# Kernel optimization log

Measured on AMD Instinct MI355X. Metric: run time of the kernel, lower is better.

The kernel has to match this reference:

```python
import jax, jax.numpy as jnp
import numpy as np

N, E = 50000, 800000
IN_C, HID, HEADS, LAT = 128, 64, 2, 32
NEG_SLOPE = 0.2  # PyG GATConv default LeakyReLU slope


def gat_layer(x, src, dst, W, att_src, att_dst, bias, heads, out_ch, concat, n):
    # Linear projection, per-head: [n, heads, out_ch]
    h = (x @ W).reshape(n, heads, out_ch)
    a_src = jnp.einsum('nhc,hc->nh', h, att_src)  # [n, heads]
    a_dst = jnp.einsum('nhc,hc->nh', h, att_dst)
    # Per-edge attention logits (edge j->i uses src j, dst i)
    alpha = jax.nn.leaky_relu(a_src[src] + a_dst[dst], negative_slope=NEG_SLOPE)  # [e, heads]
    # Segment softmax over incoming edges of each destination node
    amax = jax.ops.segment_max(alpha, dst, num_segments=n)
    ealpha = jnp.exp(alpha - amax[dst])
    denom = jax.ops.segment_sum(ealpha, dst, num_segments=n)
    alpha = ealpha / (denom[dst] + 1e-16)
    # Weighted scatter-aggregate of source features
    msg = h[src] * alpha[:, :, None]  # [e, heads, out_ch]
    out = jax.ops.segment_sum(msg, dst, num_segments=n)  # [n, heads, out_ch]
    out = out.reshape(n, heads * out_ch) if concat else out.mean(axis=1)
    return out + bias


def setup_inputs() -> dict:
    key = jax.random.key(0)
    ks = jax.random.split(key, 16)
    x = jax.random.normal(ks[0], (N, IN_C), dtype=jnp.float32)
    edge_index = jax.random.randint(ks[1], (2, E), 0, N, dtype=jnp.int32).astype(jnp.int64)
    s = 0.1
    W1 = jax.random.normal(ks[2], (IN_C, HEADS * HID), dtype=jnp.float32) * s
    att_src1 = jax.random.normal(ks[3], (HEADS, HID), dtype=jnp.float32) * s
    att_dst1 = jax.random.normal(ks[4], (HEADS, HID), dtype=jnp.float32) * s
    b1 = jnp.zeros((HEADS * HID,), dtype=jnp.float32)
    Wmu = jax.random.normal(ks[5], (HEADS * HID, LAT), dtype=jnp.float32) * s
    att_src_mu = jax.random.normal(ks[6], (1, LAT), dtype=jnp.float32) * s
    att_dst_mu = jax.random.normal(ks[7], (1, LAT), dtype=jnp.float32) * s
    bmu = jnp.zeros((LAT,), dtype=jnp.float32)
    Wlv = jax.random.normal(ks[8], (HEADS * HID, LAT), dtype=jnp.float32) * s
    att_src_lv = jax.random.normal(ks[9], (1, LAT), dtype=jnp.float32) * s
    att_dst_lv = jax.random.normal(ks[10], (1, LAT), dtype=jnp.float32) * s
    blv = jnp.zeros((LAT,), dtype=jnp.float32)
    return {"x": x, "edge_index": edge_index, "W1": W1, "att_src1": att_src1,
            "att_dst1": att_dst1, "b1": b1, "Wmu": Wmu, "att_src_mu": att_src_mu,
            "att_dst_mu": att_dst_mu, "bmu": bmu, "Wlv": Wlv,
            "att_src_lv": att_src_lv, "att_dst_lv": att_dst_lv, "blv": blv}


def reference(x, edge_index, W1, att_src1, att_dst1, b1,
              Wmu, att_src_mu, att_dst_mu, bmu,
              Wlv, att_src_lv, att_dst_lv, blv):
    n = x.shape[0]
    # PyG GATConv adds self-loops by default
    loops = jnp.arange(n, dtype=edge_index.dtype)
    src = jnp.concatenate([edge_index[0], loops])
    dst = jnp.concatenate([edge_index[1], loops])
    h = gat_layer(x, src, dst, W1, att_src1, att_dst1, b1, HEADS, HID, True, n)
    h = jax.nn.elu(h)
    mu = gat_layer(h, src, dst, Wmu, att_src_mu, att_dst_mu, bmu, 1, LAT, False, n)
    logvar = gat_layer(h, src, dst, Wlv, att_src_lv, att_dst_lv, blv, 1, LAT, False, n)
    return (mu, logvar)
```

## Files before the change

### kernel.cpp

```cpp
#include <hip/hip_runtime.h>
#include <hip/hip_bf16.h>

#define N_NODES 50000
#define N_EDGES 800000
#define EP (N_EDGES + N_NODES)
#define IN_C 128
#define HID 64
#define HEADS 2
#define LAT 32
#define NEG_SLOPE 0.2f
#define MAXDEG 256
#define MAXDEG1 96
#define NBUCKET 391
#define BCAP 3072
#define CHUNK 2048
#define NSCAT ((EP + CHUNK - 1) / CHUNK)
#define NPROJ1 ((N_NODES + 31) / 32)

typedef __attribute__((ext_vector_type(8))) short bf16x8;
typedef __attribute__((ext_vector_type(4))) float f32x4;

__device__ __forceinline__ unsigned short f2bf(float f) {
  unsigned u = __float_as_uint(f);
  u += 0x7FFF + ((u >> 16) & 1);
  return (unsigned short)(u >> 16);
}
__device__ __forceinline__ float bf_lo(unsigned u) { return __uint_as_float(u << 16); }
__device__ __forceinline__ float bf_hi(unsigned u) { return __uint_as_float(u & 0xFFFF0000u); }

__device__ __forceinline__ bf16x8 pack_bf8(const float* __restrict__ p) {
  float4 a = *(const float4*)p;
  float4 b = *(const float4*)(p + 4);
  bf16x8 r;
  r[0] = (short)f2bf(a.x); r[1] = (short)f2bf(a.y);
  r[2] = (short)f2bf(a.z); r[3] = (short)f2bf(a.w);
  r[4] = (short)f2bf(b.x); r[5] = (short)f2bf(b.y);
  r[6] = (short)f2bf(b.z); r[7] = (short)f2bf(b.w);
  return r;
}

__global__ __launch_bounds__(256) void prep_kernel(
    const float* __restrict__ W1, const float* __restrict__ Wmu,
    const float* __restrict__ Wlv, int* __restrict__ cursor,
    unsigned short* __restrict__ Wb1g, unsigned short* __restrict__ Wb2g) {
  const int b = blockIdx.x, t = threadIdx.x;
  if (b == 0) {
    for (int i = t; i < NBUCKET; i += 256) cursor[i] = 0;
  } else if (b <= 64) {
    int i = (b - 1) * 256 + t;
    int k = i >> 7, n = i & 127;
    int kk = k >> 5, q = (k >> 3) & 3, j = k & 7;
    Wb1g[((((kk << 2) + q) << 7) + n) * 8 + j] = f2bf(W1[i]);
  } else {
    int i = (b - 65) * 256 + t;
    int k = i >> 6, n = i & 63;
    float v = (n < 32) ? Wmu[k * 32 + n] : Wlv[k * 32 + (n - 32)];
    int kk = k >> 5, q = (k >> 3) & 3, j = k & 7;
    Wb2g[((((kk << 2) + q) << 6) + n) * 8 + j] = f2bf(v);
  }
}

struct ScatSmem {
  int histL[512];
  int baseL[512];
  int gbaseL[512];
  int wsumS[4];
  int nvalS;
  unsigned staging[CHUNK];
  unsigned short bktidL[CHUNK];
};
struct Proj1Smem {
  float part[32][4];
  unsigned short xs[32][136];
};
union K1Smem { ScatSmem sc; Proj1Smem p1; };

__global__ __launch_bounds__(256) void k1_kernel(
    const int* __restrict__ ei, int* __restrict__ cursor,
    unsigned* __restrict__ csr,
    const float* __restrict__ x, const unsigned short* __restrict__ Wb1g,
    const float* __restrict__ att_src, const float* __restrict__ att_dst,
    unsigned short* __restrict__ h1b, float* __restrict__ a1) {
  __shared__ K1Smem sm;
  const int t = threadIdx.x, lane = t & 63, wid = t >> 6;

  if (blockIdx.x < NSCAT) {
    for (int i = t; i < 512; i += 256) sm.sc.histL[i] = 0;
    __syncthreads();
    int myb[CHUNK / 256];
    int myloc[CHUNK / 256];
    unsigned mypay[CHUNK / 256];
    #pragma unroll
    for (int i = 0; i < CHUNK / 256; ++i) {
      int e = blockIdx.x * CHUNK + i * 256 + t;
      if (e < EP) {
        int s, d;
        if (e < N_EDGES) { s = ei[e]; d = ei[N_EDGES + e]; }
        else { s = d = e - N_EDGES; }
        int b = d >> 7;
        myb[i] = b;
        mypay[i] = ((unsigned)(d & 127) << 17) | (unsigned)s;
        myloc[i] = atomicAdd(&sm.sc.histL[b], 1);
      } else myb[i] = -1;
    }
    __syncthreads();
    {
      int v0 = sm.sc.histL[2 * t], v1 = sm.sc.histL[2 * t + 1];
      int pair = v0 + v1, inc = pair;
      #pragma unroll
      for (int off = 1; off < 64; off <<= 1) {
        int nv = __shfl_up(inc, off);
        if (lane >= off) inc += nv;
      }
      if (lane == 63) sm.sc.wsumS[wid] = inc;
      __syncthreads();
      if (t == 0) {
        int run = 0;
        #pragma unroll
        for (int w = 0; w < 4; ++w) { int c = sm.sc.wsumS[w]; sm.sc.wsumS[w] = run; run += c; }
        sm.sc.nvalS = run;
      }
      __syncthreads();
      int excl = sm.sc.wsumS[wid] + inc - pair;
      sm.sc.baseL[2 * t] = excl;
      sm.sc.baseL[2 * t + 1] = excl + v0;
    }
    __syncthreads();
    #pragma unroll
    for (int i = 0; i < CHUNK / 256; ++i)
      if (myb[i] >= 0) {
        int p = sm.sc.baseL[myb[i]] + myloc[i];
        sm.sc.staging[p] = mypay[i];
        sm.sc.bktidL[p] = (unsigned short)myb[i];
      }
    for (int b = t; b < NBUCKET; b += 256) {
      int c = sm.sc.histL[b];
      sm.sc.gbaseL[b] = c ? atomicAdd(&cursor[b], c) : 0;
    }
    __syncthreads();
    const int nval = sm.sc.nvalS;
    for (int j = t; j < nval; j += 256) {
      int b = sm.sc.bktidL[j];
      int off = sm.sc.gbaseL[b] + (j - sm.sc.baseL[b]);
      if (off < BCAP) csr[b * BCAP + off] = sm.sc.staging[j];
    }
  } else {
    const int pb = blockIdx.x - NSCAT;
    const int row0 = pb * 32;
    if (t < 128) ((float*)sm.p1.part)[t] = 0.f;
    {
      int row = t >> 3;
      int col0 = (t & 7) * 16;
      int gr = row0 + row; if (gr >= N_NODES) gr = N_NODES - 1;
      const float* xp = x + (size_t)gr * 128 + col0;
      *(bf16x8*)&sm.p1.xs[row][col0]     = pack_bf8(xp);
      *(bf16x8*)&sm.p1.xs[row][col0 + 8] = pack_bf8(xp + 8);
    }
    __syncthreads();
    const int w = wid;
    const int m = lane & 15, quad = lane >> 4;
    const int n0 = w * 32;
    const int head = w >> 1;
    f32x4 acc[2][2] = {};
    #pragma unroll
    for (int kk = 0; kk < 4; ++kk) {
      bf16x8 afr[2], bfr[2];
      #pragma unroll
      for (int mt = 0; mt < 2; ++mt)
        afr[mt] = *(const bf16x8*)&sm.p1.xs[mt * 16 + m][kk * 32 + quad * 8];
      #pragma unroll
      for (int nt = 0; nt < 2; ++nt)
        bfr[nt] = *(const bf16x8*)&Wb1g[((((kk << 2) + quad) << 7) + n0 + nt * 16 + m) * 8];
      #pragma unroll
      for (int mt = 0; mt < 2; ++mt)
        #pragma unroll
        for (int nt = 0; nt < 2; ++nt)
          acc[mt][nt] = __builtin_amdgcn_mfma_f32_16x16x32_bf16(
              afr[mt], bfr[nt], acc[mt][nt], 0, 0, 0);
    }
    float asv[2], adv[2];
    #pragma unroll
    for (int nt = 0; nt < 2; ++nt) {
      int cc = ((n0 & 63) + nt * 16 + m);
      asv[nt] = att_src[head * HID + cc];
      adv[nt] = att_dst[head * HID + cc];
    }
    #pragma unroll
    for (int mt = 0; mt < 2; ++mt)
      #pragma unroll
      for (int r = 0; r < 4; ++r) {
        int row = row0 + mt * 16 + quad * 4 + r;
        if (row < N_NODES) {
          #pragma unroll
          for (int nt = 0; nt < 2; ++nt)
            h1b[(size_t)row * 128 + n0 + nt * 16 + m] = f2bf(acc[mt][nt][r]);
        }
        float s = acc[mt][0][r] * asv[0] + acc[mt][1][r] * asv[1];
        float d = acc[mt][0][r] * adv[0] + acc[mt][1][r] * adv[1];
        #pragma unroll
        for (int off = 8; off; off >>= 1) {
          s += __shfl_xor(s, off);
          d += __shfl_xor(d, off);
        }
        if (m == 0) {
          atomicAdd(&sm.p1.part[mt * 16 + quad * 4 + r][head], s);
          atomicAdd(&sm.p1.part[mt * 16 + quad * 4 + r][2 + head], d);
        }
      }
    __syncthreads();
    if (t < 32) {
      int row = row0 + t;
      if (row < N_NODES)
        *(float4*)&a1[(size_t)row * 4] = make_float4(
            sm.p1.part[t][0], sm.p1.part[t][1], sm.p1.part[t][2], sm.p1.part[t][3]);
    }
  }
}

__global__ __launch_bounds__(256) void bucket_fill_kernel(
    const int* __restrict__ cursor, unsigned* __restrict__ csr,
    int* __restrict__ counts, int* __restrict__ cend) {
  __shared__ unsigned eseg[BCAP];
  __shared__ int hist[128];
  __shared__ int basef[128];
  __shared__ int cur[128];
  const int b = blockIdx.x, t = threadIdx.x;
  const int segbase = b * BCAP;
  int cnt = cursor[b];
  if (cnt > BCAP) cnt = BCAP;
  if (t < 128) hist[t] = 0;
  __syncthreads();
  for (int j = t; j < cnt; j += 256) {
    unsigned u = csr[segbase + j];
    eseg[j] = u;
    atomicAdd(&hist[u >> 17], 1);
  }
  __syncthreads();
  if (t < 64) {
    int v0 = hist[2 * t], v1 = hist[2 * t + 1];
    int pair = v0 + v1, inc = pair;
    #pragma unroll
    for (int off = 1; off < 64; off <<= 1) {
      int nv = __shfl_up(inc, off);
      if (t >= off) inc += nv;
    }
    int excl = inc - pair;
    basef[2 * t] = excl;
    basef[2 * t + 1] = excl + v0;
  }
  __syncthreads();
  if (t < 128) {
    cur[t] = basef[t];
    int n = b * 128 + t;
    if (n < N_NODES) {
      counts[n] = hist[t];
      cend[n] = segbase + basef[t] + hist[t];
    }
  }
  __syncthreads();
  for (int j = t; j < cnt; j += 256) {
    unsigned u = eseg[j];
    int dl = u >> 17;
    int p = atomicAdd(&cur[dl], 1);
    csr[segbase + p] = u & 0x1FFFF;
  }
}

__global__ __launch_bounds__(256) void agg1_proj2_kernel(
    const int* __restrict__ counts, const int* __restrict__ cend,
    const unsigned* __restrict__ csr_src, const float4* __restrict__ a1,
    const unsigned* __restrict__ h1b2, const float* __restrict__ b,
    const unsigned short* __restrict__ Wb2g,
    const float* __restrict__ asmu, const float* __restrict__ admu,
    const float* __restrict__ aslv, const float* __restrict__ adlv,
    unsigned short* __restrict__ h2b, float* __restrict__ a2) {
  __shared__ __align__(16) float2 w_lds[16][MAXDEG1];
  __shared__ __align__(16) unsigned short s_lds[16][MAXDEG1];
  __shared__ __align__(16) unsigned short hrow[16][136];
  __shared__ __align__(16) float sm_a2[16][4];
  const int t = threadIdx.x, wid = t >> 6, lane = t & 63;
  if (t < 64) ((float*)sm_a2)[t] = 0.f;
  const int nbase = blockIdx.x * 16;

  int cnt_r[4];
  float p0r[4], p1r[4];
  #pragma unroll
  for (int nd = 0; nd < 4; ++nd) {
    const int slot = wid * 4 + nd;
    const int n = nbase + slot;
    const int end = cend[n];
    int cnt = counts[n]; if (cnt > MAXDEG1) cnt = MAXDEG1;
    const int beg = end - cnt;
    cnt_r[nd] = cnt;
    const float4 bv = a1[n];
    float p0 = 0.f, p1 = 0.f;
    for (int i = lane; i < cnt; i += 64) {
      int s = (int)csr_src[beg + i];
      float4 av = a1[s];
      float l0 = av.x + bv.z; l0 = l0 > 0.f ? l0 : NEG_SLOPE * l0;
      float l1 = av.y + bv.w; l1 = l1 > 0.f ? l1 : NEG_SLOPE * l1;
      float e0 = __expf(l0), e1 = __expf(l1);
      w_lds[slot][i] = make_float2(e0, e1);
      s_lds[slot][i] = (unsigned short)s;
      p0 += e0; p1 += e1;
    }
    #pragma unroll
    for (int off = 32; off; off >>= 1) {
      p0 += __shfl_xor(p0, off);
      p1 += __shfl_xor(p1, off);
    }
    p0r[nd] = p0; p1r[nd] = p1;
  }

  const int g = lane >> 4, lq = lane & 15, head = lq >> 3;
  #pragma unroll
  for (int nd = 0; nd < 4; ++nd) {
    const int slot = wid * 4 + nd;
    const int cnt = cnt_r[nd];
    float acc[8] = {0.f, 0.f, 0.f, 0.f, 0.f, 0.f, 0.f, 0.f};
    #pragma unroll 4
    for (int i = g; i < cnt; i += 4) {
      int s = (int)s_lds[slot][i];
      float w = ((const float*)&w_lds[slot][i])[head];
      uint4 u = *(const uint4*)(h1b2 + (size_t)s * 64 + lq * 4);
      acc[0] += bf_lo(u.x) * w; acc[1] += bf_hi(u.x) * w;
      acc[2] += bf_lo(u.y) * w; acc[3] += bf_hi(u.y) * w;
      acc[4] += bf_lo(u.z) * w; acc[5] += bf_hi(u.z) * w;
      acc[6] += bf_lo(u.w) * w; acc[7] += bf_hi(u.w) * w;
    }
    #pragma unroll
    for (int jj = 0; jj < 8; ++jj) {
      acc[jj] += __shfl_xor(acc[jj], 16);
      acc[jj] += __shfl_xor(acc[jj], 32);
    }
    if (g == 0) {
      float inv = 1.f / ((head ? p1r[nd] : p0r[nd]) + 1e-16f);
      bf16x8 o;
      #pragma unroll
      for (int jj = 0; jj < 8; ++jj) {
        float v = acc[jj] * inv + b[lq * 8 + jj];
        v = v > 0.f ? v : (__expf(v) - 1.f);
        o[jj] = (short)f2bf(v);
      }
      *(bf16x8*)&hrow[slot][lq * 8] = o;
    }
  }
  __syncthreads();

  const int m = lane & 15, quad = lane >> 4;
  const int c = wid * 16 + m;
  const int j = wid >> 1;
  f32x4 acc2 = {};
  #pragma unroll
  for (int kk = 0; kk < 4; ++kk) {
    bf16x8 af = *(const bf16x8*)&hrow[m][kk * 32 + quad * 8];
    bf16x8 bf = *(const bf16x8*)&Wb2g[((((kk << 2) + quad) << 6) + c) * 8];
    acc2 = __builtin_amdgcn_mfma_f32_16x16x32_bf16(af, bf, acc2, 0, 0, 0);
  }
  const float asv = (j ? aslv : asmu)[(wid & 1) * 16 + m];
  const float adv = (j ? adlv : admu)[(wid & 1) * 16 + m];
  #pragma unroll
  for (int r = 0; r < 4; ++r) {
    const int slot = quad * 4 + r;
    h2b[(size_t)(nbase + slot) * 64 + c] = f2bf(acc2[r]);
    float s = acc2[r] * asv, d = acc2[r] * adv;
    #pragma unroll
    for (int off = 8; off; off >>= 1) {
      s += __shfl_xor(s, off);
      d += __shfl_xor(d, off);
    }
    if (m == 0) {
      atomicAdd(&sm_a2[slot][j * 2 + 0], s);
      atomicAdd(&sm_a2[slot][j * 2 + 1], d);
    }
  }
  __syncthreads();
  if (t < 16)
    *(float4*)&a2[(size_t)(nbase + t) * 4] = make_float4(
        sm_a2[t][0], sm_a2[t][1], sm_a2[t][2], sm_a2[t][3]);
}

__global__ __launch_bounds__(256) void agg2_csr_kernel(
    const int* __restrict__ counts, const int* __restrict__ cend,
    const unsigned* __restrict__ csr_src, const float4* __restrict__ a2,
    const unsigned* __restrict__ h2b2,
    const float* __restrict__ bmu, const float* __restrict__ blv,
    float* __restrict__ out) {
  __shared__ float2 w_lds[4][MAXDEG];
  __shared__ int   s_lds[4][MAXDEG];
  const int t = threadIdx.x, wid = t >> 6, lane = t & 63;
  const int n = blockIdx.x * 4 + wid;
  const int end = cend[n];
  int cnt = counts[n];
  if (cnt > MAXDEG) cnt = MAXDEG;
  const int beg = end - cnt;
  const float4 bv = a2[n];
  float p0 = 0.f, p1 = 0.f;
  for (int i = lane; i < cnt; i += 64) {
    int s = (int)csr_src[beg + i];
    float4 av = a2[s];
    float l0 = av.x + bv.y; l0 = l0 > 0.f ? l0 : NEG_SLOPE * l0;
    float l1 = av.z + bv.w; l1 = l1 > 0.f ? l1 : NEG_SLOPE * l1;
    float e0 = expf(l0), e1 = expf(l1);
    w_lds[wid][i] = make_float2(e0, e1);
    s_lds[wid][i] = s;
    p0 += e0; p1 += e1;
  }
  #pragma unroll
  for (int off = 32; off; off >>= 1) {
    p0 += __shfl_xor(p0, off);
    p1 += __shfl_xor(p1, off);
  }
  __syncthreads();
  const int g = lane >> 3;
  const int lq = lane & 7;
  const int j = lq >> 2;
  float acc[8] = {0.f, 0.f, 0.f, 0.f, 0.f, 0.f, 0.f, 0.f};
  #pragma unroll 2
  for (int i = g; i < cnt; i += 8) {
    int s = s_lds[wid][i];
    float w = ((const float*)&w_lds[wid][i])[j];
    uint4 u = *(const uint4*)(h2b2 + (size_t)s * 32 + lq * 4);
    acc[0] += bf_lo(u.x) * w; acc[1] += bf_hi(u.x) * w;
    acc[2] += bf_lo(u.y) * w; acc[3] += bf_hi(u.y) * w;
    acc[4] += bf_lo(u.z) * w; acc[5] += bf_hi(u.z) * w;
    acc[6] += bf_lo(u.w) * w; acc[7] += bf_hi(u.w) * w;
  }
  #pragma unroll
  for (int jj = 0; jj < 8; ++jj) {
    acc[jj] += __shfl_xor(acc[jj], 8);
    acc[jj] += __shfl_xor(acc[jj], 16);
    acc[jj] += __shfl_xor(acc[jj], 32);
  }
  if (g == 0) {
    float inv = 1.f / ((j ? p1 : p0) + 1e-16f);
    const float* bb = j ? blv : bmu;
    const int o = (lq & 3) * 8;
    float r[8];
    #pragma unroll
    for (int jj = 0; jj < 8; ++jj) r[jj] = acc[jj] * inv + bb[o + jj];
    float4* dst = (float4*)(out + (size_t)j * N_NODES * LAT + (size_t)n * LAT + o);
    dst[0] = make_float4(r[0], r[1], r[2], r[3]);
    dst[1] = make_float4(r[4], r[5], r[6], r[7]);
  }
}

extern "C" void kernel_launch(void* const* d_in, const int* in_sizes, int n_in,
                              void* d_out, int out_size, void* d_ws, size_t ws_size,
                              hipStream_t stream) {
  const float* x        = (const float*)d_in[0];
  const int* ei         = (const int*)d_in[1];
  const float* W1       = (const float*)d_in[2];
  const float* att_src1 = (const float*)d_in[3];
  const float* att_dst1 = (const float*)d_in[4];
  const float* b1       = (const float*)d_in[5];
  const float* Wmu      = (const float*)d_in[6];
  const float* asmu     = (const float*)d_in[7];
  const float* admu     = (const float*)d_in[8];
  const float* bmu      = (const float*)d_in[9];
  const float* Wlv      = (const float*)d_in[10];
  const float* aslv     = (const float*)d_in[11];
  const float* adlv     = (const float*)d_in[12];
  const float* blv      = (const float*)d_in[13];
  float* out = (float*)d_out;

  float* ws   = (float*)d_ws;
  float* hact = ws;
  float* a1   = hact + (size_t)N_NODES * 128;
  float* a2   = a1 + (size_t)N_NODES * 4;
  unsigned short* h1b = (unsigned short*)(a2 + (size_t)N_NODES * 4);
  unsigned short* h2b = h1b + (size_t)N_NODES * 128;
  unsigned short* Wb1g = h2b + (size_t)N_NODES * 64;
  unsigned short* Wb2g = Wb1g + 16384;
  int* counts = (int*)(Wb2g + 8192);
  int* cend   = counts + N_NODES;
  int* cursor = cend + N_NODES;
  unsigned* csr = (unsigned*)(cursor + NBUCKET);

  prep_kernel<<<97, 256, 0, stream>>>(W1, Wmu, Wlv, cursor, Wb1g, Wb2g);

  k1_kernel<<<NSCAT + NPROJ1, 256, 0, stream>>>(
      ei, cursor, csr, x, Wb1g, att_src1, att_dst1, h1b, a1);
  bucket_fill_kernel<<<NBUCKET, 256, 0, stream>>>(cursor, csr, counts, cend);
  agg1_proj2_kernel<<<N_NODES / 16, 256, 0, stream>>>(
      counts, cend, csr, (const float4*)a1, (const unsigned*)h1b, b1,
      Wb2g, asmu, admu, aslv, adlv, h2b, a2);
  agg2_csr_kernel<<<N_NODES / 4, 256, 0, stream>>>(
      counts, cend, csr, (const float4*)a2, (const unsigned*)h2b, bmu, blv, out);
}
```

Before: 203.6 us.

## Fuse bucket fill into agg1 kernel and emit fixed-stride ushort CSR

Removes the separate bucket_fill kernel. Each agg1 block now scans its whole 128-node bucket segment and keeps the edges for its own 16 nodes in shared memory, then writes per-node counts and a fixed-stride 16-bit source list for the layer-2 kernel. This saves one launch and a read-modify-write pass over the CSR. In exchange, each bucket segment is read 8 times (once per 16-node block), and layer 2 now caps degree at 96 instead of 256. Layer 2 also switches to the fast __expf.

```diff
diff --git a/kernel.cpp b/kernel.cpp
--- a/kernel.cpp
+++ b/kernel.cpp
@@ -9,7 +9,6 @@
 #define HEADS 2
 #define LAT 32
 #define NEG_SLOPE 0.2f
-#define MAXDEG 256
 #define MAXDEG1 96
 #define NBUCKET 391
 #define BCAP 3072
@@ -217,70 +216,49 @@
   }
 }
 
-__global__ __launch_bounds__(256) void bucket_fill_kernel(
-    const int* __restrict__ cursor, unsigned* __restrict__ csr,
-    int* __restrict__ counts, int* __restrict__ cend) {
-  __shared__ unsigned eseg[BCAP];
-  __shared__ int hist[128];
-  __shared__ int basef[128];
-  __shared__ int cur[128];
-  const int b = blockIdx.x, t = threadIdx.x;
-  const int segbase = b * BCAP;
-  int cnt = cursor[b];
-  if (cnt > BCAP) cnt = BCAP;
-  if (t < 128) hist[t] = 0;
-  __syncthreads();
-  for (int j = t; j < cnt; j += 256) {
-    unsigned u = csr[segbase + j];
-    eseg[j] = u;
-    atomicAdd(&hist[u >> 17], 1);
-  }
-  __syncthreads();
-  if (t < 64) {
-    int v0 = hist[2 * t], v1 = hist[2 * t + 1];
-    int pair = v0 + v1, inc = pair;
-    #pragma unroll
-    for (int off = 1; off < 64; off <<= 1) {
-      int nv = __shfl_up(inc, off);
-      if (t >= off) inc += nv;
-    }
-    int excl = inc - pair;
-    basef[2 * t] = excl;
-    basef[2 * t + 1] = excl + v0;
-  }
-  __syncthreads();
-  if (t < 128) {
-    cur[t] = basef[t];
-    int n = b * 128 + t;
-    if (n < N_NODES) {
-      counts[n] = hist[t];
-      cend[n] = segbase + basef[t] + hist[t];
-    }
-  }
-  __syncthreads();
-  for (int j = t; j < cnt; j += 256) {
-    unsigned u = eseg[j];
-    int dl = u >> 17;
-    int p = atomicAdd(&cur[dl], 1);
-    csr[segbase + p] = u & 0x1FFFF;
-  }
-}
-
 __global__ __launch_bounds__(256) void agg1_proj2_kernel(
-    const int* __restrict__ counts, const int* __restrict__ cend,
-    const unsigned* __restrict__ csr_src, const float4* __restrict__ a1,
+    const int* __restrict__ cursor, const unsigned* __restrict__ csr_stg,
+    const float4* __restrict__ a1,
     const unsigned* __restrict__ h1b2, const float* __restrict__ b,
     const unsigned short* __restrict__ Wb2g,
     const float* __restrict__ asmu, const float* __restrict__ admu,
     const float* __restrict__ aslv, const float* __restrict__ adlv,
-    unsigned short* __restrict__ h2b, float* __restrict__ a2) {
+    unsigned short* __restrict__ h2b, float* __restrict__ a2,
+    int* __restrict__ counts, unsigned short* __restrict__ csr2) {
   __shared__ __align__(16) float2 w_lds[16][MAXDEG1];
   __shared__ __align__(16) unsigned short s_lds[16][MAXDEG1];
   __shared__ __align__(16) unsigned short hrow[16][136];
   __shared__ __align__(16) float sm_a2[16][4];
+  __shared__ int lcnt[16];
   const int t = threadIdx.x, wid = t >> 6, lane = t & 63;
   if (t < 64) ((float*)sm_a2)[t] = 0.f;
+  if (t < 16) lcnt[t] = 0;
   const int nbase = blockIdx.x * 16;
+  const int bkt = nbase >> 7;
+  const int lo = nbase & 127;
+  __syncthreads();
+
+  int cnt_b = cursor[bkt]; if (cnt_b > BCAP) cnt_b = BCAP;
+  const unsigned* seg = csr_stg + (size_t)bkt * BCAP;
+  for (int i = t; i < cnt_b; i += 256) {
+    unsigned u = seg[i];
+    int rel = (int)(u >> 17) - lo;
+    if ((unsigned)rel < 16u) {
+      int p = atomicAdd(&lcnt[rel], 1);
+      if (p < MAXDEG1) s_lds[rel][p] = (unsigned short)(u & 0x1FFFF);
+    }
+  }
+  __syncthreads();
+
+  if (t < 16) {
+    int c = lcnt[t]; if (c > MAXDEG1) c = MAXDEG1;
+    counts[nbase + t] = c;
+  }
+  for (int i = t; i < 16 * MAXDEG1; i += 256) {
+    int slot = i / MAXDEG1, idx = i - slot * MAXDEG1;
+    int c = lcnt[slot]; if (c > MAXDEG1) c = MAXDEG1;
+    if (idx < c) csr2[(size_t)(nbase + slot) * MAXDEG1 + idx] = s_lds[slot][idx];
+  }
 
   int cnt_r[4];
   float p0r[4], p1r[4];
@@ -288,20 +266,17 @@
   for (int nd = 0; nd < 4; ++nd) {
     const int slot = wid * 4 + nd;
     const int n = nbase + slot;
-    const int end = cend[n];
-    int cnt = counts[n]; if (cnt > MAXDEG1) cnt = MAXDEG1;
-    const int beg = end - cnt;
+    int cnt = lcnt[slot]; if (cnt > MAXDEG1) cnt = MAXDEG1;
     cnt_r[nd] = cnt;
     const float4 bv = a1[n];
     float p0 = 0.f, p1 = 0.f;
     for (int i = lane; i < cnt; i += 64) {
-      int s = (int)csr_src[beg + i];
+      int s = (int)s_lds[slot][i];
       float4 av = a1[s];
       float l0 = av.x + bv.z; l0 = l0 > 0.f ? l0 : NEG_SLOPE * l0;
       float l1 = av.y + bv.w; l1 = l1 > 0.f ? l1 : NEG_SLOPE * l1;
       float e0 = __expf(l0), e1 = __expf(l1);
       w_lds[slot][i] = make_float2(e0, e1);
-      s_lds[slot][i] = (unsigned short)s;
       p0 += e0; p1 += e1;
     }
     #pragma unroll
@@ -381,29 +356,26 @@
 }
 
 __global__ __launch_bounds__(256) void agg2_csr_kernel(
-    const int* __restrict__ counts, const int* __restrict__ cend,
-    const unsigned* __restrict__ csr_src, const float4* __restrict__ a2,
-    const unsigned* __restrict__ h2b2,
+    const int* __restrict__ counts, const unsigned short* __restrict__ csr2,
+    const float4* __restrict__ a2, const unsigned* __restrict__ h2b2,
     const float* __restrict__ bmu, const float* __restrict__ blv,
     float* __restrict__ out) {
-  __shared__ float2 w_lds[4][MAXDEG];
-  __shared__ int   s_lds[4][MAXDEG];
+  __shared__ float2 w_lds[4][MAXDEG1];
+  __shared__ unsigned short s_lds[4][MAXDEG1];
   const int t = threadIdx.x, wid = t >> 6, lane = t & 63;
   const int n = blockIdx.x * 4 + wid;
-  const int end = cend[n];
-  int cnt = counts[n];
-  if (cnt > MAXDEG) cnt = MAXDEG;
-  const int beg = end - cnt;
+  const int cnt = counts[n];
+  const unsigned short* lst = csr2 + (size_t)n * MAXDEG1;
   const float4 bv = a2[n];
   float p0 = 0.f, p1 = 0.f;
   for (int i = lane; i < cnt; i += 64) {
-    int s = (int)csr_src[beg + i];
+    int s = (int)lst[i];
     float4 av = a2[s];
     float l0 = av.x + bv.y; l0 = l0 > 0.f ? l0 : NEG_SLOPE * l0;
     float l1 = av.z + bv.w; l1 = l1 > 0.f ? l1 : NEG_SLOPE * l1;
-    float e0 = expf(l0), e1 = expf(l1);
+    float e0 = __expf(l0), e1 = __expf(l1);
     w_lds[wid][i] = make_float2(e0, e1);
-    s_lds[wid][i] = s;
+    s_lds[wid][i] = (unsigned short)s;
     p0 += e0; p1 += e1;
   }
   #pragma unroll
@@ -418,7 +390,7 @@
   float acc[8] = {0.f, 0.f, 0.f, 0.f, 0.f, 0.f, 0.f, 0.f};
   #pragma unroll 2
   for (int i = g; i < cnt; i += 8) {
-    int s = s_lds[wid][i];
+    int s = (int)s_lds[wid][i];
     float w = ((const float*)&w_lds[wid][i])[j];
     uint4 u = *(const uint4*)(h2b2 + (size_t)s * 32 + lq * 4);
     acc[0] += bf_lo(u.x) * w; acc[1] += bf_hi(u.x) * w;
@@ -465,8 +437,8 @@
   float* out = (float*)d_out;
 
   float* ws   = (float*)d_ws;
-  float* hact = ws;
-  float* a1   = hact + (size_t)N_NODES * 128;
+  unsigned short* csr2 = (unsigned short*)ws;
+  float* a1   = ws + (size_t)N_NODES * 128;
   float* a2   = a1 + (size_t)N_NODES * 4;
   unsigned short* h1b = (unsigned short*)(a2 + (size_t)N_NODES * 4);
   unsigned short* h2b = h1b + (size_t)N_NODES * 128;
@@ -481,10 +453,9 @@
 
   k1_kernel<<<NSCAT + NPROJ1, 256, 0, stream>>>(
       ei, cursor, csr, x, Wb1g, att_src1, att_dst1, h1b, a1);
-  bucket_fill_kernel<<<NBUCKET, 256, 0, stream>>>(cursor, csr, counts, cend);
   agg1_proj2_kernel<<<N_NODES / 16, 256, 0, stream>>>(
-      counts, cend, csr, (const float4*)a1, (const unsigned*)h1b, b1,
-      Wb2g, asmu, admu, aslv, adlv, h2b, a2);
+      cursor, csr, (const float4*)a1, (const unsigned*)h1b, b1,
+      Wb2g, asmu, admu, aslv, adlv, h2b, a2, counts, csr2);
   agg2_csr_kernel<<<N_NODES / 4, 256, 0, stream>>>(
-      counts, cend, csr, (const float4*)a2, (const unsigned*)h2b, bmu, blv, out);
-}
+      counts, csr2, (const float4*)a2, (const unsigned*)h2b, bmu, blv, out);
+}
```

Result: no change. 205.2 us (+0.7%).
